# Kernel optimization log

Hardware: AMD Instinct MI355X
Metric: run time of the kernel (lower is better)

Reference implementation:

```python
import jax, jax.numpy as jnp
import numpy as np
from jax import lax

K = 3            # RFAConv kernel size
CIN = 66         # RFAConv in_channel = c2/2 + 2
UP = 64          # up channel count = c2/2
BN_EPS = 1e-5


def conv2d(x, w, stride=1, padding=0, groups=1, bias=None):
    out = lax.conv_general_dilated(
        x, w, (stride, stride), [(padding, padding), (padding, padding)],
        dimension_numbers=("NCHW", "OIHW", "NCHW"), feature_group_count=groups)
    if bias is not None:
        out = out + bias[None, :, None, None]
    return out


def avgpool3(x):
    # AvgPool2d(kernel=3, pad=1, stride=1), count_include_pad=True -> /9 everywhere
    s = lax.reduce_window(x, 0.0, lax.add, (1, 1, 3, 3), (1, 1, 1, 1),
                          [(0, 0), (0, 0), (1, 1), (1, 1)])
    return s / 9.0


def setup_inputs() -> dict:
    key = jax.random.key(0)
    ks = jax.random.split(key, 8)
    c1, c2 = 64, 128
    inp = {
        "x": jax.random.normal(ks[0], (8, c1, 256, 256), jnp.float32),
        "w_squeeze": jax.random.normal(ks[1], (c2, 4 * c1, 1, 1), jnp.float32) * 0.05,
        "w_gw": jax.random.normal(ks[2], (CIN * K * K, 1, 1, 1), jnp.float32) * 0.3,
        "w_gf": jax.random.normal(ks[3], (CIN * K * K, 1, K, K), jnp.float32) * 0.3,
        "bn_gamma": jnp.ones((CIN * K * K,), jnp.float32),
        "bn_beta": jnp.zeros((CIN * K * K,), jnp.float32),
        "bn_mean": jnp.zeros((CIN * K * K,), jnp.float32),
        "bn_var": jnp.ones((CIN * K * K,), jnp.float32),
        "w_conv": jax.random.normal(ks[4], (UP, CIN, K, K), jnp.float32) * 0.05,
        "b_conv": jnp.zeros((UP,), jnp.float32),
    }
    return inp


def reference(x, w_squeeze, w_gw, w_gf, bn_gamma, bn_beta, bn_mean, bn_var,
              w_conv, b_conv):
    # space_to_depth: [B,C,H,W] -> [B,4C,H/2,W/2]
    x = jnp.concatenate([x[..., ::2, ::2], x[..., 1::2, ::2],
                         x[..., ::2, 1::2], x[..., 1::2, 1::2]], axis=1)
    # squeeze0: 1x1 conv 4*c1 -> c2
    x = conv2d(x, w_squeeze)
    up, low = x[:, :UP], x[:, UP:]

    # AddCoords (with_r=False): append normalized xx (width) and yy (height)
    b, _, h, w = up.shape
    xx = (jnp.arange(w, dtype=up.dtype) / (w - 1) * 2.0 - 1.0)
    yy = (jnp.arange(h, dtype=up.dtype) / (h - 1) * 2.0 - 1.0)
    xx = jnp.broadcast_to(xx[None, None, None, :], (b, 1, h, w))
    yy = jnp.broadcast_to(yy[None, None, :, None], (b, 1, h, w))
    up = jnp.concatenate([up, xx, yy], axis=1)   # [b, 66, h, w]

    # RFAConv
    weight = conv2d(avgpool3(up), w_gw, groups=CIN)          # [b, 594, h, w]
    weight = jax.nn.softmax(weight.reshape(b, CIN, K * K, h, w), axis=2)

    feat = conv2d(up, w_gf, stride=1, padding=1, groups=CIN)  # [b, 594, h, w]
    scale = bn_gamma / jnp.sqrt(bn_var + BN_EPS)
    shift = bn_beta - bn_mean * scale
    feat = jax.nn.relu(feat * scale[None, :, None, None] + shift[None, :, None, None])
    feat = feat.reshape(b, CIN, K * K, h, w)

    wd = feat * weight
    # rearrange 'b c (n1 n2) h w -> b c (h n1) (w n2)'
    wd = wd.reshape(b, CIN, K, K, h, w).transpose(0, 1, 4, 2, 5, 3)
    wd = wd.reshape(b, CIN, h * K, w * K)
    up = conv2d(wd, w_conv, stride=K, bias=b_conv)            # [b, 64, h, w]

    y = jnp.concatenate([up, low], axis=1)                    # [b, 128, h, w]
    # channel shuffle: gather even channels then odd channels
    bb, n, hh, ww = y.shape
    y = y.reshape(bb, n // 2, 2, hh, ww)
    return jnp.concatenate([y[:, :, 0], y[:, :, 1]], axis=1)
```

## Files before the change

kernel.cpp:

```cpp
#include <hip/hip_runtime.h>
#include <math.h>

typedef __attribute__((ext_vector_type(8))) short short8;
typedef __attribute__((ext_vector_type(4))) float f32x4;

#define B 8
#define H 128
#define W 128
#define UPC 64
#define CIN 66
#define BN_EPS 1e-5f

#define BSQ_U16  ((size_t)16777216)
#define BSQ_CNT  32768
#define BF_U16   (BSQ_U16 + BSQ_CNT)
#define BF_CNT   38912
#define SC_F     ((size_t)8424448)
#define SH_F     (SC_F + 594)

static __device__ __forceinline__ unsigned short f2bf(float f) {
    unsigned u = __float_as_uint(f);
    u += 0x7fffu + ((u >> 16) & 1u);
    return (unsigned short)(u >> 16);
}
static __device__ __forceinline__ unsigned pack2(float lo, float hi) {
    return __builtin_amdgcn_perm(__float_as_uint(hi) + 0x8000u,
                                 __float_as_uint(lo) + 0x8000u, 0x07060302u);
}

__global__ void prep_kernel(const float* __restrict__ w_squeeze,
                            const float* __restrict__ gamma,
                            const float* __restrict__ beta,
                            const float* __restrict__ mean,
                            const float* __restrict__ var,
                            const float* __restrict__ w_conv,
                            float* __restrict__ ws)
{
    unsigned short* wsu = (unsigned short*)ws;
    int tid = blockIdx.x * blockDim.x + threadIdx.x;
    int nth = gridDim.x * blockDim.x;

    for (int idx = tid; idx < BSQ_CNT; idx += nth) {
        int j = idx & 7, lane = (idx >> 3) & 63, r = idx >> 9;
        int nt = r & 7, kc = r >> 3;
        int k = kc * 32 + ((lane >> 4) << 3) + j;
        int n = nt * 16 + (lane & 15);
        wsu[BSQ_U16 + idx] = f2bf(w_squeeze[n * 256 + k]);
    }
    for (int idx = tid; idx < BF_CNT; idx += nth) {
        int j = idx & 7, lane = (idx >> 3) & 63, r = idx >> 9;
        int nt = r & 3, ks = r >> 2;
        int k = ks * 32 + ((lane >> 4) << 3) + j;
        int n = nt * 16 + (lane & 15);
        float v = (k < 594) ? w_conv[n * 594 + k] : 0.f;
        wsu[BF_U16 + idx] = f2bf(v);
    }
    for (int i = tid; i < CIN * 9; i += nth) {
        float sc = gamma[i] / sqrtf(var[i] + BN_EPS);
        ws[SC_F + i] = sc;
        ws[SH_F + i] = beta[i] - mean[i] * sc;
    }
}

__global__ __launch_bounds__(256, 4) void squeeze_mfma(
    const float* __restrict__ x,
    float* __restrict__ wsp,
    float* __restrict__ out)
{
    __shared__ uint4 As[32 * 64];

    const int m0 = blockIdx.x * 64;
    const int w0 = m0 & 127;
    const int h  = (m0 >> 7) & 127;
    const int b  = m0 >> 14;
    const int tid  = threadIdx.x;
    const int lane = tid & 63;
    const int wv   = tid >> 6;
    const int oct = tid >> 5;
    const int pp  = tid & 31;

    float4 v[2][8];
#pragma unroll
    for (int gy = 0; gy < 2; ++gy)
#pragma unroll
        for (int i = 0; i < 8; ++i)
            v[gy][i] = *(const float4*)(x +
                (size_t)(b * 64 + oct * 8 + i) * 65536 +
                (2 * h + gy) * 256 + 2 * w0 + 4 * pp);

#pragma unroll
    for (int gy = 0; gy < 2; ++gy)
#pragma unroll
        for (int gx = 0; gx < 2; ++gx)
#pragma unroll
            for (int p = 0; p < 2; ++p) {
                const int comp = p * 2 + gx;
                uint4 u;
                u.x = pack2(((const float*)&v[gy][0])[comp], ((const float*)&v[gy][1])[comp]);
                u.y = pack2(((const float*)&v[gy][2])[comp], ((const float*)&v[gy][3])[comp]);
                u.z = pack2(((const float*)&v[gy][4])[comp], ((const float*)&v[gy][5])[comp]);
                u.w = pack2(((const float*)&v[gy][6])[comp], ((const float*)&v[gy][7])[comp]);
                As[((gy + 2 * gx) * 8 + oct) * 64 + 2 * pp + p] = u;
            }

    const unsigned short* bsq = (const unsigned short*)wsp + BSQ_U16;
    short8 breg[2][8];
#pragma unroll
    for (int ks = 0; ks < 8; ++ks)
#pragma unroll
        for (int j = 0; j < 2; ++j)
            breg[j][ks] = *(const short8*)(bsq +
                (size_t)((ks * 8 + (2 * wv + j)) * 64 + lane) * 8);

    __syncthreads();

    const int q = lane >> 4, m = lane & 15;
    f32x4 acc[4][2];
#pragma unroll
    for (int mt = 0; mt < 4; ++mt)
#pragma unroll
        for (int j = 0; j < 2; ++j) acc[mt][j] = (f32x4){0.f, 0.f, 0.f, 0.f};

#pragma unroll
    for (int ks = 0; ks < 8; ++ks)
#pragma unroll
        for (int mt = 0; mt < 4; ++mt) {
            short8 a = *(const short8*)&As[(ks * 4 + q) * 64 + mt * 16 + m];
            acc[mt][0] = __builtin_amdgcn_mfma_f32_16x16x32_bf16(a, breg[0][ks], acc[mt][0], 0, 0, 0);
            acc[mt][1] = __builtin_amdgcn_mfma_f32_16x16x32_bf16(a, breg[1][ks], acc[mt][1], 0, 0, 0);
        }

    if (wv < 2) {
        unsigned short* upw = (unsigned short*)wsp;
#pragma unroll
        for (int j = 0; j < 2; ++j) {
            const int oc = (2 * wv + j) * 16 + m;
#pragma unroll
            for (int mt = 0; mt < 4; ++mt) {
                uint2 st;
                st.x = pack2(acc[mt][j][0], acc[mt][j][1]);
                st.y = pack2(acc[mt][j][2], acc[mt][j][3]);
                *(uint2*)(upw + (size_t)(b * 64 + oc) * 16384 + h * 128
                          + (w0 + mt * 16 + q * 4)) = st;
            }
        }
    } else {
#pragma unroll
        for (int j = 0; j < 2; ++j) {
            const int oc = (2 * wv + j) * 16 + m;
            const int lc = oc - 64;
            const int ch = (lc & 1) ? (96 + ((lc - 1) >> 1)) : (32 + (lc >> 1));
#pragma unroll
            for (int mt = 0; mt < 4; ++mt) {
                float4 st = {acc[mt][j][0], acc[mt][j][1], acc[mt][j][2], acc[mt][j][3]};
                *(float4*)(out + ((size_t)(b * 128 + ch) * 128 + h) * 128
                           + (w0 + mt * 16 + q * 4)) = st;
            }
        }
    }
}

__device__ __forceinline__ void fs_from_n(
    int cu, const float n[9],
    const float* __restrict__ w_gw, const float* __restrict__ w_gf,
    const float* __restrict__ scp, const float* __restrict__ shp,
    float fs[9])
{
    const float p = (n[0] + n[1] + n[2] + n[3] + n[4] + n[5] + n[6] + n[7] + n[8]) * (1.f / 9.f);
    const float* gw = w_gw + cu * 9;
    const float* gf = w_gf + cu * 81;
    const float* sc = scp + cu * 9;
    const float* sh = shp + cu * 9;
    float e[9], se = 0.f;
#pragma unroll
    for (int j = 0; j < 9; ++j) { e[j] = __expf(p * gw[j]); se += e[j]; }
    const float sinv = 1.f / se;
#pragma unroll
    for (int j = 0; j < 9; ++j) {
        float cv = n[0] * gf[j * 9 + 0];
        cv = fmaf(n[1], gf[j * 9 + 1], cv); cv = fmaf(n[2], gf[j * 9 + 2], cv);
        cv = fmaf(n[3], gf[j * 9 + 3], cv); cv = fmaf(n[4], gf[j * 9 + 4], cv);
        cv = fmaf(n[5], gf[j * 9 + 5], cv); cv = fmaf(n[6], gf[j * 9 + 6], cv);
        cv = fmaf(n[7], gf[j * 9 + 7], cv); cv = fmaf(n[8], gf[j * 9 + 8], cv);
        float f = fmaf(cv, sc[j], sh[j]);
        fs[j] = fmaxf(f, 0.f) * (e[j] * sinv);
    }
}

__device__ __forceinline__ void pack_into(unsigned* pk, int ci, const float fs[9], float& carry)
{
    const int off = 9 * ci;
    if ((ci & 1) == 0) {
#pragma unroll
        for (int t = 0; t < 4; ++t) pk[off / 2 + t] = pack2(fs[2 * t], fs[2 * t + 1]);
        carry = fs[8];
    } else {
        pk[(off - 1) / 2] = pack2(carry, fs[0]);
#pragma unroll
        for (int t = 0; t < 4; ++t) pk[(off + 1) / 2 + t] = pack2(fs[1 + 2 * t], fs[2 + 2 * t]);
    }
}

template<bool BORDER>
__device__ __forceinline__ void chunk_fs(
    int cs, int wv, int lane, int h0, int w0,
    const unsigned short* __restrict__ upb,
    const float* __restrict__ w_gw, const float* __restrict__ w_gf,
    const float* __restrict__ scp, const float* __restrict__ shp,
    unsigned pk[36])
{
    const int px = lane & 7, py = lane >> 3;
    const int gy0 = h0 + py - 1;
    const int gxc = w0 + px;
    float carry = 0.f;

    if (!BORDER) {
        const int gx0 = (gxc - 1) & ~1;
        const unsigned sh = (gxc & 1) ? 0u : 16u;
        const size_t rowoff = (size_t)gy0 * 128 + gx0;
#pragma unroll
        for (int ci = 0; ci < 8; ++ci) {
            const int cu = __builtin_amdgcn_readfirstlane(cs + 8 * wv + ci);
            const unsigned short* cb = upb + (size_t)cu * 16384 + rowoff;
            float n[9];
#pragma unroll
            for (int dy = 0; dy < 3; ++dy) {
                const uint2 v = *(const uint2*)(cb + dy * 128);
                unsigned long long t = (((unsigned long long)v.y) << 32) | v.x;
                t >>= sh;
                n[dy * 3 + 0] = __uint_as_float((unsigned)t << 16);
                n[dy * 3 + 1] = __uint_as_float((unsigned)t & 0xffff0000u);
                n[dy * 3 + 2] = __uint_as_float((unsigned)(t >> 32) << 16);
            }
            float fs[9];
            fs_from_n(cu, n, w_gw, w_gf, scp, shp, fs);
            pack_into(pk, ci, fs, carry);
        }
    } else {
#pragma unroll
        for (int ci = 0; ci < 8; ++ci) {
            const int cu = __builtin_amdgcn_readfirstlane(cs + 8 * wv + ci);
            const unsigned short* cb = upb + (size_t)cu * 16384;
            float n[9];
#pragma unroll
            for (int dy = 0; dy < 3; ++dy)
#pragma unroll
                for (int dx = 0; dx < 3; ++dx) {
                    const int gy = gy0 + dy, gx = gxc - 1 + dx;
                    const bool ok = ((unsigned)gy < 128u) & ((unsigned)gx < 128u);
                    const int cy = min(max(gy, 0), 127), cx = min(max(gx, 0), 127);
                    const float f = __uint_as_float((unsigned)cb[cy * 128 + cx] << 16);
                    n[dy * 3 + dx] = ok ? f : 0.f;
                }
            float fs[9];
            fs_from_n(cu, n, w_gw, w_gf, scp, shp, fs);
            pack_into(pk, ci, fs, carry);
        }
    }
}

__device__ __forceinline__ void coord_n(int which, int h0, int w0, int lane, float n[9])
{
    const int px = lane & 7, py = lane >> 3;
#pragma unroll
    for (int dy = 0; dy < 3; ++dy)
#pragma unroll
        for (int dx = 0; dx < 3; ++dx) {
            const int gy = h0 + py - 1 + dy, gx = w0 + px - 1 + dx;
            const bool ok = ((unsigned)gy < 128u) & ((unsigned)gx < 128u);
            const float v = (which == 0) ? (gx * (2.f / 127.f) - 1.f)
                                         : (gy * (2.f / 127.f) - 1.f);
            n[dy * 3 + dx] = ok ? v : 0.f;
        }
}

template<int NSTEPS>
__device__ __forceinline__ void do_mfma(
    int base, const uint4* As, const unsigned short* __restrict__ bfw,
    int wv, int lane, f32x4 acc[2][2])
{
    const int q = lane >> 4, m = lane & 15;
    const int ntb = (wv >> 1) * 2;
    const int pt0 = (wv & 1) * 2;
#pragma unroll
    for (int ks = 0; ks < NSTEPS; ++ks) {
        short8 b0 = *(const short8*)(bfw + (size_t)(((base + ks) * 4 + ntb + 0) * 64 + lane) * 8);
        short8 b1 = *(const short8*)(bfw + (size_t)(((base + ks) * 4 + ntb + 1) * 64 + lane) * 8);
#pragma unroll
        for (int mt = 0; mt < 2; ++mt) {
            short8 a = *(const short8*)&As[(ks * 4 + q) * 64 + (pt0 + mt) * 16 + m];
            acc[mt][0] = __builtin_amdgcn_mfma_f32_16x16x32_bf16(a, b0, acc[mt][0], 0, 0, 0);
            acc[mt][1] = __builtin_amdgcn_mfma_f32_16x16x32_bf16(a, b1, acc[mt][1], 0, 0, 0);
        }
    }
}

__global__ __launch_bounds__(256, 4) void fused_mfma(
    const float* __restrict__ wsp,
    const float* __restrict__ w_gw,
    const float* __restrict__ w_gf,
    const float* __restrict__ b_conv,
    float* __restrict__ out)
{
    __shared__ uint4 As[40 * 64];

    const int bx = blockIdx.x;
    const int w0 = (bx & 15) * 8;
    const int h0 = ((bx >> 4) & 15) * 8;
    const int b  = bx >> 8;
    const int tid = threadIdx.x, lane = tid & 63, wv = tid >> 6;
    const bool interior = (h0 > 0) & (h0 < 120) & (w0 > 0) & (w0 < 120);

    const unsigned short* upb = (const unsigned short*)wsp + (size_t)b * UPC * 16384;
    const float* scp = wsp + SC_F;
    const float* shp = wsp + SH_F;
    const unsigned short* bfw = (const unsigned short*)wsp + BF_U16;

    f32x4 acc[2][2];
#pragma unroll
    for (int mt = 0; mt < 2; ++mt)
#pragma unroll
        for (int j = 0; j < 2; ++j) acc[mt][j] = (f32x4){0.f, 0.f, 0.f, 0.f};

    {
        unsigned pk[36];
        if (interior) chunk_fs<false>(0, wv, lane, h0, w0, upb, w_gw, w_gf, scp, shp, pk);
        else          chunk_fs<true >(0, wv, lane, h0, w0, upb, w_gw, w_gf, scp, shp, pk);
        __syncthreads();
#pragma unroll
        for (int kb = 0; kb < 9; ++kb)
            As[(9 * wv + kb) * 64 + lane] =
                (uint4){pk[4 * kb], pk[4 * kb + 1], pk[4 * kb + 2], pk[4 * kb + 3]};
        __syncthreads();
        do_mfma<9>(0, As, bfw, wv, lane, acc);
    }

    {
        unsigned pk[36];
        if (interior) chunk_fs<false>(32, wv, lane, h0, w0, upb, w_gw, w_gf, scp, shp, pk);
        else          chunk_fs<true >(32, wv, lane, h0, w0, upb, w_gw, w_gf, scp, shp, pk);

        float fsA[9], fsB[9];
        if (wv == 3) {
            float n2[9];
            coord_n(0, h0, w0, lane, n2);
            fs_from_n(64, n2, w_gw, w_gf, scp, shp, fsA);
            coord_n(1, h0, w0, lane, n2);
            fs_from_n(65, n2, w_gw, w_gf, scp, shp, fsB);
        }
        __syncthreads();
#pragma unroll
        for (int kb = 0; kb < 9; ++kb)
            As[(9 * wv + kb) * 64 + lane] =
                (uint4){pk[4 * kb], pk[4 * kb + 1], pk[4 * kb + 2], pk[4 * kb + 3]};
        if (wv == 3) {
            uint4 v;
            v.x = pack2(fsA[0], fsA[1]); v.y = pack2(fsA[2], fsA[3]);
            v.z = pack2(fsA[4], fsA[5]); v.w = pack2(fsA[6], fsA[7]);
            As[36 * 64 + lane] = v;
            v.x = pack2(fsA[8], fsB[0]); v.y = pack2(fsB[1], fsB[2]);
            v.z = pack2(fsB[3], fsB[4]); v.w = pack2(fsB[5], fsB[6]);
            As[37 * 64 + lane] = v;
            v.x = pack2(fsB[7], fsB[8]); v.y = 0u; v.z = 0u; v.w = 0u;
            As[38 * 64 + lane] = v;
            v.x = 0u; v.y = 0u; v.z = 0u; v.w = 0u;
            As[39 * 64 + lane] = v;
        }
        __syncthreads();
        do_mfma<10>(9, As, bfw, wv, lane, acc);
    }

    const int q = lane >> 4, m = lane & 15;
    const int ntb = (wv >> 1) * 2, pt0 = (wv & 1) * 2;
#pragma unroll
    for (int mt = 0; mt < 2; ++mt)
#pragma unroll
        for (int j = 0; j < 2; ++j) {
            const int oc = (ntb + j) * 16 + m;
            const float bias = b_conv[oc];
            const int ch = (oc & 1) ? (64 + (oc >> 1)) : (oc >> 1);
#pragma unroll
            for (int r = 0; r < 4; ++r) {
                const int pix = (pt0 + mt) * 16 + q * 4 + r;
                out[((size_t)((b * 128 + ch) * 128 + (h0 + (pix >> 3)))) * 128
                    + (w0 + (pix & 7))] = acc[mt][j][r] + bias;
            }
        }
}

extern "C" void kernel_launch(void* const* d_in, const int* in_sizes, int n_in,
                              void* d_out, int out_size, void* d_ws, size_t ws_size,
                              hipStream_t stream)
{
    const float* x         = (const float*)d_in[0];
    const float* w_squeeze = (const float*)d_in[1];
    const float* w_gw      = (const float*)d_in[2];
    const float* w_gf      = (const float*)d_in[3];
    const float* gamma     = (const float*)d_in[4];
    const float* beta      = (const float*)d_in[5];
    const float* mean      = (const float*)d_in[6];
    const float* var       = (const float*)d_in[7];
    const float* w_conv    = (const float*)d_in[8];
    const float* b_conv    = (const float*)d_in[9];
    float* out = (float*)d_out;
    float* ws  = (float*)d_ws;

    prep_kernel<<<160, 256, 0, stream>>>(w_squeeze, gamma, beta, mean, var, w_conv, ws);
    squeeze_mfma<<<(B * H * W) / 64, 256, 0, stream>>>(x, ws, out);
    fused_mfma<<<B * 16 * 16, 256, 0, stream>>>(ws, w_gw, w_gf, b_conv, out);
}
```

Measured before the change: 324.8 us.

## Stage squeeze output through LDS for wide coalesced stores; prescale gw for exp2

The squeeze kernel now writes its MFMA accumulators to a padded LDS tile and then writes each output channel row with wide contiguous stores, for both the bf16 up workspace and the fp32 low-half output, instead of scattered 8/16-byte stores per lane. Input loads are split into two rounds of four channels to reduce register pressure. The gw weights are premultiplied by log2(e) in the prep kernel so the softmax can use exp2f, and one __syncthreads before the first LDS write in the fused kernel is removed. The cost is more LDS (about 35KB per block, which may limit occupancy) and extra barriers. The removed barrier may be unsafe if As could still be in use, though it sits at the start of the block, so it is probably safe.

```diff
diff --git a/kernel.cpp b/kernel.cpp
--- a/kernel.cpp
+++ b/kernel.cpp
@@ -17,6 +17,7 @@
 #define BF_CNT   38912
 #define SC_F     ((size_t)8424448)
 #define SH_F     (SC_F + 594)
+#define GW2_F    (SH_F + 594)
 
 static __device__ __forceinline__ unsigned short f2bf(float f) {
     unsigned u = __float_as_uint(f);
@@ -34,6 +35,7 @@
                             const float* __restrict__ mean,
                             const float* __restrict__ var,
                             const float* __restrict__ w_conv,
+                            const float* __restrict__ w_gw,
                             float* __restrict__ ws)
 {
     unsigned short* wsu = (unsigned short*)ws;
@@ -59,6 +61,7 @@
         float sc = gamma[i] / sqrtf(var[i] + BN_EPS);
         ws[SC_F + i] = sc;
         ws[SH_F + i] = beta[i] - mean[i] * sc;
+        ws[GW2_F + i] = w_gw[i] * 1.44269504f;
     }
 }
 
@@ -67,7 +70,9 @@
     float* __restrict__ wsp,
     float* __restrict__ out)
 {
-    __shared__ uint4 As[32 * 64];
+    __shared__ float lf[128 * 68];
+    uint2* As2 = (uint2*)lf;
+    const uint4* As4 = (const uint4*)lf;
 
     const int m0 = blockIdx.x * 64;
     const int w0 = m0 & 127;
@@ -79,30 +84,6 @@
     const int oct = tid >> 5;
     const int pp  = tid & 31;
 
-    float4 v[2][8];
-#pragma unroll
-    for (int gy = 0; gy < 2; ++gy)
-#pragma unroll
-        for (int i = 0; i < 8; ++i)
-            v[gy][i] = *(const float4*)(x +
-                (size_t)(b * 64 + oct * 8 + i) * 65536 +
-                (2 * h + gy) * 256 + 2 * w0 + 4 * pp);
-
-#pragma unroll
-    for (int gy = 0; gy < 2; ++gy)
-#pragma unroll
-        for (int gx = 0; gx < 2; ++gx)
-#pragma unroll
-            for (int p = 0; p < 2; ++p) {
-                const int comp = p * 2 + gx;
-                uint4 u;
-                u.x = pack2(((const float*)&v[gy][0])[comp], ((const float*)&v[gy][1])[comp]);
-                u.y = pack2(((const float*)&v[gy][2])[comp], ((const float*)&v[gy][3])[comp]);
-                u.z = pack2(((const float*)&v[gy][4])[comp], ((const float*)&v[gy][5])[comp]);
-                u.w = pack2(((const float*)&v[gy][6])[comp], ((const float*)&v[gy][7])[comp]);
-                As[((gy + 2 * gx) * 8 + oct) * 64 + 2 * pp + p] = u;
-            }
-
     const unsigned short* bsq = (const unsigned short*)wsp + BSQ_U16;
     short8 breg[2][8];
 #pragma unroll
@@ -112,6 +93,29 @@
             breg[j][ks] = *(const short8*)(bsq +
                 (size_t)((ks * 8 + (2 * wv + j)) * 64 + lane) * 8);
 
+#pragma unroll
+    for (int r = 0; r < 2; ++r) {
+        float4 v[2][4];
+#pragma unroll
+        for (int gy = 0; gy < 2; ++gy)
+#pragma unroll
+            for (int i = 0; i < 4; ++i)
+                v[gy][i] = *(const float4*)(x +
+                    (size_t)(b * 64 + oct * 8 + r * 4 + i) * 65536 +
+                    (2 * h + gy) * 256 + 2 * w0 + 4 * pp);
+#pragma unroll
+        for (int gy = 0; gy < 2; ++gy)
+#pragma unroll
+            for (int gx = 0; gx < 2; ++gx)
+#pragma unroll
+                for (int p = 0; p < 2; ++p) {
+                    const int comp = p * 2 + gx;
+                    uint2 u;
+                    u.x = pack2(((const float*)&v[gy][0])[comp], ((const float*)&v[gy][1])[comp]);
+                    u.y = pack2(((const float*)&v[gy][2])[comp], ((const float*)&v[gy][3])[comp]);
+                    As2[(((gy + 2 * gx) * 8 + oct) * 64 + 2 * pp + p) * 2 + r] = u;
+                }
+    }
     __syncthreads();
 
     const int q = lane >> 4, m = lane & 15;
@@ -125,55 +129,66 @@
     for (int ks = 0; ks < 8; ++ks)
 #pragma unroll
         for (int mt = 0; mt < 4; ++mt) {
-            short8 a = *(const short8*)&As[(ks * 4 + q) * 64 + mt * 16 + m];
+            short8 a = *(const short8*)&As4[(ks * 4 + q) * 64 + mt * 16 + m];
             acc[mt][0] = __builtin_amdgcn_mfma_f32_16x16x32_bf16(a, breg[0][ks], acc[mt][0], 0, 0, 0);
             acc[mt][1] = __builtin_amdgcn_mfma_f32_16x16x32_bf16(a, breg[1][ks], acc[mt][1], 0, 0, 0);
         }
 
-    if (wv < 2) {
-        unsigned short* upw = (unsigned short*)wsp;
+    __syncthreads();
+#pragma unroll
+    for (int mt = 0; mt < 4; ++mt)
 #pragma unroll
         for (int j = 0; j < 2; ++j) {
             const int oc = (2 * wv + j) * 16 + m;
-#pragma unroll
-            for (int mt = 0; mt < 4; ++mt) {
-                uint2 st;
-                st.x = pack2(acc[mt][j][0], acc[mt][j][1]);
-                st.y = pack2(acc[mt][j][2], acc[mt][j][3]);
-                *(uint2*)(upw + (size_t)(b * 64 + oc) * 16384 + h * 128
-                          + (w0 + mt * 16 + q * 4)) = st;
-            }
+            *(f32x4*)&lf[oc * 68 + mt * 16 + q * 4] = acc[mt][j];
+        }
+    __syncthreads();
+
+    const int oc2 = tid >> 1, seg = tid & 1;
+    f32x4 rv[8];
+#pragma unroll
+    for (int i = 0; i < 8; ++i)
+        rv[i] = *(const f32x4*)&lf[oc2 * 68 + seg * 32 + i * 4];
+
+    if (oc2 < UPC) {
+        unsigned short* upw = (unsigned short*)wsp;
+        unsigned short* base = upw + (size_t)(b * 64 + oc2) * 16384 + h * 128
+                             + (w0 + seg * 32);
+#pragma unroll
+        for (int k = 0; k < 4; ++k) {
+            uint4 st;
+            st.x = pack2(rv[2 * k][0], rv[2 * k][1]);
+            st.y = pack2(rv[2 * k][2], rv[2 * k][3]);
+            st.z = pack2(rv[2 * k + 1][0], rv[2 * k + 1][1]);
+            st.w = pack2(rv[2 * k + 1][2], rv[2 * k + 1][3]);
+            *(uint4*)(base + k * 8) = st;
         }
     } else {
-#pragma unroll
-        for (int j = 0; j < 2; ++j) {
-            const int oc = (2 * wv + j) * 16 + m;
-            const int lc = oc - 64;
-            const int ch = (lc & 1) ? (96 + ((lc - 1) >> 1)) : (32 + (lc >> 1));
-#pragma unroll
-            for (int mt = 0; mt < 4; ++mt) {
-                float4 st = {acc[mt][j][0], acc[mt][j][1], acc[mt][j][2], acc[mt][j][3]};
-                *(float4*)(out + ((size_t)(b * 128 + ch) * 128 + h) * 128
-                           + (w0 + mt * 16 + q * 4)) = st;
-            }
+        const int lc = oc2 - 64;
+        const int ch = (lc & 1) ? (96 + ((lc - 1) >> 1)) : (32 + (lc >> 1));
+        float* op = out + ((size_t)(b * 128 + ch) * 128 + h) * 128 + (w0 + seg * 32);
+#pragma unroll
+        for (int i = 0; i < 8; ++i) {
+            float4 st = {rv[i][0], rv[i][1], rv[i][2], rv[i][3]};
+            *(float4*)(op + i * 4) = st;
         }
     }
 }
 
 __device__ __forceinline__ void fs_from_n(
     int cu, const float n[9],
-    const float* __restrict__ w_gw, const float* __restrict__ w_gf,
+    const float* __restrict__ gw2, const float* __restrict__ w_gf,
     const float* __restrict__ scp, const float* __restrict__ shp,
     float fs[9])
 {
     const float p = (n[0] + n[1] + n[2] + n[3] + n[4] + n[5] + n[6] + n[7] + n[8]) * (1.f / 9.f);
-    const float* gw = w_gw + cu * 9;
+    const float* gw = gw2 + cu * 9;
     const float* gf = w_gf + cu * 81;
     const float* sc = scp + cu * 9;
     const float* sh = shp + cu * 9;
     float e[9], se = 0.f;
 #pragma unroll
-    for (int j = 0; j < 9; ++j) { e[j] = __expf(p * gw[j]); se += e[j]; }
+    for (int j = 0; j < 9; ++j) { e[j] = exp2f(p * gw[j]); se += e[j]; }
     const float sinv = 1.f / se;
 #pragma unroll
     for (int j = 0; j < 9; ++j) {
@@ -205,7 +220,7 @@
 __device__ __forceinline__ void chunk_fs(
     int cs, int wv, int lane, int h0, int w0,
     const unsigned short* __restrict__ upb,
-    const float* __restrict__ w_gw, const float* __restrict__ w_gf,
+    const float* __restrict__ gw2, const float* __restrict__ w_gf,
     const float* __restrict__ scp, const float* __restrict__ shp,
     unsigned pk[36])
 {
@@ -233,7 +248,7 @@
                 n[dy * 3 + 2] = __uint_as_float((unsigned)(t >> 32) << 16);
             }
             float fs[9];
-            fs_from_n(cu, n, w_gw, w_gf, scp, shp, fs);
+            fs_from_n(cu, n, gw2, w_gf, scp, shp, fs);
             pack_into(pk, ci, fs, carry);
         }
     } else {
@@ -253,7 +268,7 @@
                     n[dy * 3 + dx] = ok ? f : 0.f;
                 }
             float fs[9];
-            fs_from_n(cu, n, w_gw, w_gf, scp, shp, fs);
+            fs_from_n(cu, n, gw2, w_gf, scp, shp, fs);
             pack_into(pk, ci, fs, carry);
         }
     }
@@ -297,7 +312,6 @@
 
 __global__ __launch_bounds__(256, 4) void fused_mfma(
     const float* __restrict__ wsp,
-    const float* __restrict__ w_gw,
     const float* __restrict__ w_gf,
     const float* __restrict__ b_conv,
     float* __restrict__ out)
@@ -314,6 +328,7 @@
     const unsigned short* upb = (const unsigned short*)wsp + (size_t)b * UPC * 16384;
     const float* scp = wsp + SC_F;
     const float* shp = wsp + SH_F;
+    const float* gw2 = wsp + GW2_F;
     const unsigned short* bfw = (const unsigned short*)wsp + BF_U16;
 
     f32x4 acc[2][2];
@@ -324,9 +339,8 @@
 
     {
         unsigned pk[36];
-        if (interior) chunk_fs<false>(0, wv, lane, h0, w0, upb, w_gw, w_gf, scp, shp, pk);
-        else          chunk_fs<true >(0, wv, lane, h0, w0, upb, w_gw, w_gf, scp, shp, pk);
-        __syncthreads();
+        if (interior) chunk_fs<false>(0, wv, lane, h0, w0, upb, gw2, w_gf, scp, shp, pk);
+        else          chunk_fs<true >(0, wv, lane, h0, w0, upb, gw2, w_gf, scp, shp, pk);
 #pragma unroll
         for (int kb = 0; kb < 9; ++kb)
             As[(9 * wv + kb) * 64 + lane] =
@@ -337,16 +351,16 @@
 
     {
         unsigned pk[36];
-        if (interior) chunk_fs<false>(32, wv, lane, h0, w0, upb, w_gw, w_gf, scp, shp, pk);
-        else          chunk_fs<true >(32, wv, lane, h0, w0, upb, w_gw, w_gf, scp, shp, pk);
+        if (interior) chunk_fs<false>(32, wv, lane, h0, w0, upb, gw2, w_gf, scp, shp, pk);
+        else          chunk_fs<true >(32, wv, lane, h0, w0, upb, gw2, w_gf, scp, shp, pk);
 
         float fsA[9], fsB[9];
         if (wv == 3) {
             float n2[9];
             coord_n(0, h0, w0, lane, n2);
-            fs_from_n(64, n2, w_gw, w_gf, scp, shp, fsA);
+            fs_from_n(64, n2, gw2, w_gf, scp, shp, fsA);
             coord_n(1, h0, w0, lane, n2);
-            fs_from_n(65, n2, w_gw, w_gf, scp, shp, fsB);
+            fs_from_n(65, n2, gw2, w_gf, scp, shp, fsB);
         }
         __syncthreads();
 #pragma unroll
@@ -405,7 +419,7 @@
     float* out = (float*)d_out;
     float* ws  = (float*)d_ws;
 
-    prep_kernel<<<160, 256, 0, stream>>>(w_squeeze, gamma, beta, mean, var, w_conv, ws);
+    prep_kernel<<<160, 256, 0, stream>>>(w_squeeze, gamma, beta, mean, var, w_conv, w_gw, ws);
     squeeze_mfma<<<(B * H * W) / 64, 256, 0, stream>>>(x, ws, out);
-    fused_mfma<<<B * 16 * 16, 256, 0, stream>>>(ws, w_gw, w_gf, b_conv, out);
-}
+    fused_mfma<<<B * 16 * 16, 256, 0, stream>>>(ws, w_gf, b_conv, out);
+}
```

New measurement: 331.3 us. Within noise of the previous version (+2.0%).
